# Optimization experiments

Hardware: AMD Instinct MI355X
Metric: run time of the kernel (lower is better)

The kernel has to match this reference:

```python
import jax, jax.numpy as jnp
import numpy as np

H = 512
L = 4
A = 16
EPS = 1e-5


def setup_inputs() -> dict:
    key = jax.random.key(0)
    ks = jax.random.split(key, 16)
    B, S = 64, 256
    scale = 0.02
    inp = {
        "hidden": jnp.zeros((B, H), jnp.float32),
        "x": jax.random.normal(ks[0], (B, S, H), jnp.float32),
        "dones": jax.random.randint(ks[1], (B, S), 0, 2).astype(bool),
        "avail_actions": jax.random.randint(ks[2], (B, S, A), 0, 2).astype(bool),
        # MLP stack: L layers of Linear(H,H) + LayerNorm
        "Wl": jax.random.normal(ks[3], (L, H, H), jnp.float32) * scale,
        "bl": jnp.zeros((L, H), jnp.float32),
        "ln_g": jnp.ones((L, H), jnp.float32),
        "ln_b": jnp.zeros((L, H), jnp.float32),
        # GRUCell(H, H): torch layout weight_ih [3H, H] (r, z, n order)
        "W_ih": jax.random.normal(ks[4], (3 * H, H), jnp.float32) * scale,
        "W_hh": jax.random.normal(ks[5], (3 * H, H), jnp.float32) * scale,
        "b_ih": jnp.zeros((3 * H,), jnp.float32),
        "b_hh": jnp.zeros((3 * H,), jnp.float32),
        # output head
        "Wq": jax.random.normal(ks[6], (A, H), jnp.float32) * scale,
        "bq": jnp.zeros((A,), jnp.float32),
    }
    return inp


def _layer_norm(x, g, b):
    mu = jnp.mean(x, axis=-1, keepdims=True)
    var = jnp.mean(jnp.square(x - mu), axis=-1, keepdims=True)
    return (x - mu) * jax.lax.rsqrt(var + EPS) * g + b


def _gru_scan(h0, x, dones, W_ih, W_hh, b_ih, b_hh):
    # Precompute input projections for all timesteps: [B, S, 3H]
    gi = jnp.einsum("bsh,gh->bsg", x, W_ih) + b_ih
    gi_t = jnp.swapaxes(gi, 0, 1)          # [S, B, 3H]
    dones_t = jnp.swapaxes(dones, 0, 1)    # [S, B]

    def step(h, inputs):
        gi_s, done_s = inputs
        h = jnp.where(done_s[:, None], 0.0, h)  # reset carry where done
        gh = h @ W_hh.T + b_hh
        i_r, i_z, i_n = jnp.split(gi_s, 3, axis=-1)
        h_r, h_z, h_n = jnp.split(gh, 3, axis=-1)
        r = jax.nn.sigmoid(i_r + h_r)
        z = jax.nn.sigmoid(i_z + h_z)
        n = jnp.tanh(i_n + r * h_n)
        h_new = (1.0 - z) * n + z * h
        return h_new, h_new

    h_final, outs = jax.lax.scan(step, h0, (gi_t, dones_t))
    return h_final, jnp.swapaxes(outs, 0, 1)  # [B, S, H]


def reference(hidden, x, dones, avail_actions, Wl, bl, ln_g, ln_b,
              W_ih, W_hh, b_ih, b_hh, Wq, bq):
    h = x
    for l in range(L):
        h = jnp.einsum("bsh,oh->bso", h, Wl[l]) + bl[l]
        h = jax.nn.relu(_layer_norm(h, ln_g[l], ln_b[l]))
    hidden_out, rnn_out = _gru_scan(hidden, h, dones, W_ih, W_hh, b_ih, b_hh)
    q = jnp.einsum("bsh,ah->bsa", rnn_out, Wq) + bq
    unavail = 1.0 - avail_actions.astype(q.dtype)
    q = q - unavail * 1e10
    return hidden_out, q
```

## Files before the change

### kernel.cpp

```cpp
#include <hip/hip_runtime.h>
#include <hip/hip_bf16.h>

typedef short short8 __attribute__((ext_vector_type(8)));
typedef float f32x4 __attribute__((ext_vector_type(4)));

#define H 512
#define BATCH 64
#define SEQ 256
#define NROWS 16384
#define NDOM 16
#define HSTCAP 12288

__device__ __forceinline__ float bf2f(unsigned short u) {
    union { unsigned int i; float f; } v;
    v.i = ((unsigned int)u) << 16;
    return v.f;
}
__device__ __forceinline__ unsigned short f2bf(float f) {
    union { float f; unsigned int i; } v;
    v.f = f;
    unsigned int lsb = (v.i >> 16) & 1u;
    v.i += 0x7fffu + lsb;
    return (unsigned short)(v.i >> 16);
}
__device__ __forceinline__ float sigm(float x) { return 1.f / (1.f + __expf(-x)); }
__device__ __forceinline__ float tanh_fast(float x) { return 2.f / (1.f + __expf(-2.f * x)) - 1.f; }

__global__ __launch_bounds__(256) void cvt_init(
    const float* __restrict__ Wl, const float* __restrict__ Wih,
    unsigned short* __restrict__ wlb, unsigned short* __restrict__ wihb,
    unsigned int* __restrict__ meta)
{
    long idx4 = (long)blockIdx.x * 256 + threadIdx.x;
    if (idx4 < 2560) meta[idx4] = 0u;
    long i = idx4 * 4;
    const long N1 = 1048576;
    const long N2 = N1 + 786432;
    const float* src; unsigned short* dst; long off;
    if (i < N1)      { src = Wl;  dst = wlb;  off = i; }
    else if (i < N2) { src = Wih; dst = wihb; off = i - N1; }
    else return;
    float4 v = *(const float4*)(src + off);
    ushort4 o;
    o.x = f2bf(v.x); o.y = f2bf(v.y); o.z = f2bf(v.z); o.w = f2bf(v.w);
    *(ushort4*)(dst + off) = o;
}

__global__ __launch_bounds__(256) void seg_build(
    const int* __restrict__ dones, int* __restrict__ lenArr,
    unsigned int* __restrict__ hist)
{
    __shared__ int d[256];
    const int b = blockIdx.x, s = threadIdx.x;
    d[s] = dones[b * 256 + s];
    __syncthreads();
    int len = 0;
    bool start = (s == 0) || (d[s] != 0);
    if (start) {
        len = 1;
        while (s + len < 256 && d[s + len] == 0) len++;
        atomicAdd(&hist[len], 1u);
    }
    lenArr[b * 256 + s] = len;
}

__global__ __launch_bounds__(256) void seg_offsets(
    const unsigned int* __restrict__ hist, int* __restrict__ Marr,
    unsigned int* __restrict__ offs, unsigned int* __restrict__ ssum)
{
    __shared__ unsigned int h[257];
    __shared__ int Msh[257];
    const int t = threadIdx.x;
    h[t] = hist[t];
    if (t == 0) h[256] = hist[256];
    __syncthreads();
    for (int tt = t; tt <= 256; tt += 256) {
        unsigned int m = 0;
        for (int L = tt + 1; L <= 256; ++L) m += h[L];
        Marr[tt] = (int)m;
        offs[tt] = m;
        Msh[tt] = (int)m;
    }
    __syncthreads();
    if (t == 0) {
        unsigned int acc = 0;
        for (int k = 0; k <= 256; ++k) { ssum[k] = acc; acc += (unsigned int)Msh[k]; }
    }
}

__global__ __launch_bounds__(256) void seg_scatter(
    const int* __restrict__ lenArr, unsigned int* __restrict__ offs,
    int* __restrict__ recs)
{
    const int b = blockIdx.x, s = threadIdx.x;
    int len = lenArr[b * 256 + s];
    if (len > 0) {
        unsigned int pos = atomicAdd(&offs[len], 1u);
        recs[pos] = (b << 16) | s;
    }
}

__global__ __launch_bounds__(256) void pmap_build(
    const int* __restrict__ recs, const int* __restrict__ Marr,
    const unsigned int* __restrict__ ssum, const int* __restrict__ lenArr,
    int* __restrict__ pmap)
{
    const int i = blockIdx.x * 256 + threadIdx.x;
    if (i >= Marr[0]) return;
    int rec = recs[i];
    int b = rec >> 16, st = rec & 0xffff;
    int len = lenArr[b * 256 + st];
    for (int t = 0; t < len; ++t) pmap[b * 256 + st + t] = (int)ssum[t] + i;
}

__global__ __launch_bounds__(256) void h_init(
    const int* __restrict__ recs, const int* __restrict__ Marr,
    const int* __restrict__ dones, const float* __restrict__ hidden,
    unsigned short* __restrict__ hst)
{
    const int w = threadIdx.x >> 6, lane = threadIdx.x & 63;
    const int i = blockIdx.x * 4 + w;
    const int nseg = Marr[0];
    const int c0 = lane * 8;
    unsigned short* dst = hst + (long)i * 512 + c0;
    if (i < nseg) {
        int rec = recs[i];
        int b = rec >> 16, st = rec & 0xffff;
        if (st == 0 && dones[b * 256] == 0) {
            float4 va = *(const float4*)(hidden + b * 512 + c0);
            float4 vb = *(const float4*)(hidden + b * 512 + c0 + 4);
            ushort4 o0 = {f2bf(va.x), f2bf(va.y), f2bf(va.z), f2bf(va.w)};
            ushort4 o1 = {f2bf(vb.x), f2bf(vb.y), f2bf(vb.z), f2bf(vb.w)};
            *(ushort4*)dst = o0; *(ushort4*)(dst + 4) = o1;
            return;
        }
    }
    ushort4 z4 = {0, 0, 0, 0};
    *(ushort4*)dst = z4; *(ushort4*)(dst + 4) = z4;
}

__global__ __launch_bounds__(256) void mlp_gi(
    const float* __restrict__ x,
    const unsigned short* __restrict__ wlb,
    const unsigned short* __restrict__ wihb,
    const float* __restrict__ bl,
    const float* __restrict__ lng,
    const float* __restrict__ lnb,
    const float* __restrict__ bih,
    const int* __restrict__ pmap,
    unsigned short* __restrict__ gi)
{
    __shared__ unsigned short ldsAct[64 * 512];
    __shared__ unsigned short ldsW[512 * 64];
    __shared__ float red[64 * 8];
    const int tid = threadIdx.x;
    const int lane = tid & 63;
    const int w = tid >> 6;
    const long m0 = (long)blockIdx.x * 64;

#pragma unroll
    for (int it = 0; it < 16; ++it) {
        int ch = it * 256 + tid;
        int row = ch >> 6;
        int c = ch & 63;
        const float* xp = x + (m0 + row) * 512 + c * 8;
        float4 a = *(const float4*)xp;
        float4 b4 = *(const float4*)(xp + 4);
        short8 v;
        v[0] = (short)f2bf(a.x);  v[1] = (short)f2bf(a.y);
        v[2] = (short)f2bf(a.z);  v[3] = (short)f2bf(a.w);
        v[4] = (short)f2bf(b4.x); v[5] = (short)f2bf(b4.y);
        v[6] = (short)f2bf(b4.z); v[7] = (short)f2bf(b4.w);
        int byteo = (row * 1024 + c * 16) ^ ((row & 7) << 4);
        *(short8*)((char*)ldsAct + byteo) = v;
    }
    int pm[4][4];
#pragma unroll
    for (int i = 0; i < 4; ++i)
#pragma unroll
        for (int r = 0; r < 4; ++r)
            pm[i][r] = pmap[m0 + i * 16 + (lane >> 4) * 4 + r];
    __syncthreads();

    for (int l = 0; l < 4; ++l) {
        const unsigned short* W = wlb + (long)l * 512 * 512;
        f32x4 acc[4][8];
#pragma unroll
        for (int i = 0; i < 4; ++i)
#pragma unroll
            for (int jn = 0; jn < 8; ++jn) acc[i][jn] = (f32x4){0.f, 0.f, 0.f, 0.f};

        for (int kt = 0; kt < 512; kt += 64) {
            __syncthreads();
#pragma unroll
            for (int i = 0; i < 16; ++i) {
                int o = (i * 256 + tid) * 16;
                int row = o >> 7;
                int c = (o & 127) >> 4;
                long gcol = (long)kt * 2 + (long)((c ^ (row & 7)) << 4);
                __builtin_amdgcn_global_load_lds(
                    (const unsigned int*)((const char*)W + (long)row * 1024 + gcol),
                    (unsigned int*)(ldsW + (i * 256 + w * 64) * 8), 16, 0, 0);
            }
            __syncthreads();
#pragma unroll
            for (int k2 = 0; k2 < 2; ++k2) {
                short8 af[4], bfr[8];
#pragma unroll
                for (int i = 0; i < 4; ++i) {
                    int row = i * 16 + (lane & 15);
                    int byteo = (row * 1024 + kt * 2 + k2 * 64 + ((lane >> 4) * 16)) ^ ((row & 7) << 4);
                    af[i] = *(const short8*)((const char*)ldsAct + byteo);
                }
#pragma unroll
                for (int jn = 0; jn < 8; ++jn) {
                    int row = w * 128 + jn * 16 + (lane & 15);
                    int byteo = (row * 128 + k2 * 64 + ((lane >> 4) * 16)) ^ ((row & 7) << 4);
                    bfr[jn] = *(const short8*)((const char*)ldsW + byteo);
                }
#pragma unroll
                for (int i = 0; i < 4; ++i)
#pragma unroll
                    for (int jn = 0; jn < 8; ++jn)
                        acc[i][jn] = __builtin_amdgcn_mfma_f32_16x16x32_bf16(af[i], bfr[jn], acc[i][jn], 0, 0, 0);
            }
        }

        float bz[8], gl[8], bb[8];
#pragma unroll
        for (int jn = 0; jn < 8; ++jn) {
            int n = w * 128 + jn * 16 + (lane & 15);
            bz[jn] = bl[l * 512 + n]; gl[jn] = lng[l * 512 + n]; bb[jn] = lnb[l * 512 + n];
        }
#pragma unroll
        for (int i = 0; i < 4; ++i)
#pragma unroll
            for (int jn = 0; jn < 8; ++jn)
#pragma unroll
                for (int r = 0; r < 4; ++r) acc[i][jn][r] += bz[jn];

#pragma unroll
        for (int i = 0; i < 4; ++i) {
#pragma unroll
            for (int r = 0; r < 4; ++r) {
                float sv = 0.f, qv = 0.f;
#pragma unroll
                for (int jn = 0; jn < 8; ++jn) {
                    float v = acc[i][jn][r];
                    sv += v; qv += v * v;
                }
                sv += __shfl_xor(sv, 1); qv += __shfl_xor(qv, 1);
                sv += __shfl_xor(sv, 2); qv += __shfl_xor(qv, 2);
                sv += __shfl_xor(sv, 4); qv += __shfl_xor(qv, 4);
                sv += __shfl_xor(sv, 8); qv += __shfl_xor(qv, 8);
                if ((lane & 15) == 0) {
                    int row = i * 16 + (lane >> 4) * 4 + r;
                    red[row * 8 + w * 2] = sv;
                    red[row * 8 + w * 2 + 1] = qv;
                }
            }
        }
        __syncthreads();

#pragma unroll
        for (int i = 0; i < 4; ++i) {
#pragma unroll
            for (int r = 0; r < 4; ++r) {
                int row = i * 16 + (lane >> 4) * 4 + r;
                float s_tot = red[row * 8 + 0] + red[row * 8 + 2] + red[row * 8 + 4] + red[row * 8 + 6];
                float q_tot = red[row * 8 + 1] + red[row * 8 + 3] + red[row * 8 + 5] + red[row * 8 + 7];
                float mu = s_tot * (1.f / 512.f);
                float var = q_tot * (1.f / 512.f) - mu * mu;
                float rs = rsqrtf(var + 1e-5f);
#pragma unroll
                for (int jn = 0; jn < 8; ++jn) {
                    int col = w * 128 + jn * 16 + (lane & 15);
                    float v = fmaxf(0.f, (acc[i][jn][r] - mu) * rs * gl[jn] + bb[jn]);
                    int byteo = (row * 1024 + col * 2) ^ ((row & 7) << 4);
                    *(unsigned short*)((char*)ldsAct + byteo) = f2bf(v);
                }
            }
        }
        __syncthreads();
    }

    for (int nc = 0; nc < 3; ++nc) {
        const unsigned short* W = wihb + (long)nc * 512 * 512;
        f32x4 acc[4][8];
#pragma unroll
        for (int i = 0; i < 4; ++i)
#pragma unroll
            for (int jn = 0; jn < 8; ++jn) acc[i][jn] = (f32x4){0.f, 0.f, 0.f, 0.f};

        for (int kt = 0; kt < 512; kt += 64) {
            __syncthreads();
#pragma unroll
            for (int i = 0; i < 16; ++i) {
                int o = (i * 256 + tid) * 16;
                int row = o >> 7;
                int c = (o & 127) >> 4;
                long gcol = (long)kt * 2 + (long)((c ^ (row & 7)) << 4);
                __builtin_amdgcn_global_load_lds(
                    (const unsigned int*)((const char*)W + (long)row * 1024 + gcol),
                    (unsigned int*)(ldsW + (i * 256 + w * 64) * 8), 16, 0, 0);
            }
            __syncthreads();
#pragma unroll
            for (int k2 = 0; k2 < 2; ++k2) {
                short8 af[4], bfr[8];
#pragma unroll
                for (int i = 0; i < 4; ++i) {
                    int row = i * 16 + (lane & 15);
                    int byteo = (row * 1024 + kt * 2 + k2 * 64 + ((lane >> 4) * 16)) ^ ((row & 7) << 4);
                    af[i] = *(const short8*)((const char*)ldsAct + byteo);
                }
#pragma unroll
                for (int jn = 0; jn < 8; ++jn) {
                    int row = w * 128 + jn * 16 + (lane & 15);
                    int byteo = (row * 128 + k2 * 64 + ((lane >> 4) * 16)) ^ ((row & 7) << 4);
                    bfr[jn] = *(const short8*)((const char*)ldsW + byteo);
                }
#pragma unroll
                for (int i = 0; i < 4; ++i)
#pragma unroll
                    for (int jn = 0; jn < 8; ++jn)
                        acc[i][jn] = __builtin_amdgcn_mfma_f32_16x16x32_bf16(af[i], bfr[jn], acc[i][jn], 0, 0, 0);
            }
        }

#pragma unroll
        for (int jn = 0; jn < 8; ++jn) {
            int colg = nc * 512 + w * 128 + jn * 16 + (lane & 15);
            float bz = bih[colg];
#pragma unroll
            for (int i = 0; i < 4; ++i)
#pragma unroll
                for (int r = 0; r < 4; ++r)
                    gi[(long)pm[i][r] * 1536 + colg] = f2bf(acc[i][jn][r] + bz);
        }
    }
}

__device__ __forceinline__ void dbar(unsigned int* __restrict__ dm,
                                     unsigned int epoch)
{
    __syncthreads();
    if (threadIdx.x == 0) {
        unsigned int p = __hip_atomic_fetch_add(&dm[0], 1u, __ATOMIC_RELAXED,
                                                __HIP_MEMORY_SCOPE_AGENT);
        if (p == (epoch + 1u) * 16u - 1u) {
            __hip_atomic_store(&dm[16], epoch + 1u, __ATOMIC_RELAXED,
                               __HIP_MEMORY_SCOPE_AGENT);
        } else {
            while (__hip_atomic_load(&dm[16], __ATOMIC_RELAXED,
                                     __HIP_MEMORY_SCOPE_AGENT) <= epoch)
                __builtin_amdgcn_s_sleep(2);
        }
    }
    __syncthreads();
    __builtin_amdgcn_sched_barrier(0);
}

__global__ __launch_bounds__(256, 1) void gru_seg_scan(
    const unsigned short* __restrict__ gi,
    const float* __restrict__ Whh,
    const float* __restrict__ bhh,
    const int* __restrict__ Marr,
    const unsigned int* __restrict__ ssum,
    const int* __restrict__ recs,
    unsigned short* __restrict__ hstA,
    unsigned short* __restrict__ hstB,
    unsigned short* __restrict__ rnn,
    float* __restrict__ hid_out,
    unsigned int* __restrict__ meta)
{
    __shared__ unsigned short ldsW[96 * 512];
    __shared__ int sMarr[257];
    __shared__ unsigned int sssum[257];
    const int tid = threadIdx.x;
    const int lane = tid & 63;
    const int w = tid >> 6;
    const int jg = blockIdx.x >> 4;
    const int dom = blockIdx.x & 15;
    const int j0 = jg * 32;

    for (int e = tid; e < 96 * 512; e += 256) {
        int rrow = e >> 9;
        int col = e & 511;
        int gate = rrow >> 5;
        int jl = rrow & 31;
        float v = Whh[((long)(gate * 512 + j0 + jl)) * 512 + col];
        int byteo = (rrow * 1024 + col * 2) ^ ((rrow & 7) << 4);
        *(unsigned short*)((char*)ldsW + byteo) = f2bf(v);
    }
    for (int e = tid; e < 257; e += 256) { sMarr[e] = Marr[e]; sssum[e] = ssum[e]; }

    const int jl16 = lane & 15;
    float bhr[2], bhz[2], bhn[2];
#pragma unroll
    for (int jj = 0; jj < 2; ++jj) {
        int jc = j0 + jj * 16 + jl16;
        bhr[jj] = bhh[jc]; bhz[jj] = bhh[512 + jc]; bhn[jj] = bhh[1024 + jc];
    }
    const int rbase = w * 16 + (lane >> 4) * 4;
    const int arowl = w * 16 + jl16;
    const int kcol0 = (lane >> 4) * 8;
    unsigned int* dmeta = meta + 64 * dom;
    __syncthreads();

    int crec[4], nrec[4];
    unsigned short cgr[4][2], cgz[4][2], cgn[4][2];
    unsigned short ngr[4][2], ngz[4][2], ngn[4][2];

    {
        const int Mt0 = sMarr[0];
        const long b0 = (long)sssum[0];
#pragma unroll
        for (int q = 0; q < 4; ++q) {
            int r = dom * 64 + rbase + q;
            if (r < Mt0) {
                crec[q] = recs[r];
#pragma unroll
                for (int jj = 0; jj < 2; ++jj) {
                    const unsigned short* gp = gi + (b0 + r) * 1536 + j0 + jj * 16 + jl16;
                    cgr[q][jj] = gp[0]; cgz[q][jj] = gp[512]; cgn[q][jj] = gp[1024];
                }
            } else crec[q] = -1;
        }
    }

    for (int t = 0; t < 256; ++t) {
        const int Mt = sMarr[t];
        if (Mt == 0) break;
        const int ntiles = (Mt + 63) >> 6;
        if (dom >= ntiles) break;
        const unsigned short* hsrc = (t & 1) ? hstB : hstA;
        unsigned short* hdst = (t & 1) ? hstA : hstB;
        const long base = (long)sssum[t];

        for (int tt = dom; tt < ntiles; tt += NDOM) {
            const int r0 = tt * 64;

            const unsigned short* arowp = hsrc + ((long)(r0 + arowl)) * 512 + kcol0;
            short8 af[16];
#pragma unroll
            for (int kk = 0; kk < 16; ++kk) {
                const unsigned short* ap = arowp + kk * 32;
                asm volatile("global_load_dwordx4 %0, %1, off sc0"
                             : "=v"(af[kk]) : "v"(ap));
            }
            unsigned int hu[4][2];
#pragma unroll
            for (int q = 0; q < 4; ++q)
#pragma unroll
                for (int jj = 0; jj < 2; ++jj) {
                    const unsigned short* hp = hsrc + (long)(r0 + rbase + q) * 512
                                             + j0 + jj * 16 + jl16;
                    asm volatile("global_load_ushort %0, %1, off sc0"
                                 : "=v"(hu[q][jj]) : "v"(hp));
                }
            asm volatile("s_waitcnt vmcnt(0)" ::: "memory");
            __builtin_amdgcn_sched_barrier(0);

            const bool instep = (tt + NDOM < ntiles);
            if (instep) {
#pragma unroll
                for (int q = 0; q < 4; ++q) {
                    int r = (tt + NDOM) * 64 + rbase + q;
                    if (r < Mt) {
                        nrec[q] = recs[r];
#pragma unroll
                        for (int jj = 0; jj < 2; ++jj) {
                            const unsigned short* gp = gi + (base + r) * 1536 + j0 + jj * 16 + jl16;
                            ngr[q][jj] = gp[0]; ngz[q][jj] = gp[512]; ngn[q][jj] = gp[1024];
                        }
                    } else nrec[q] = -1;
                }
            }

            f32x4 acch[3][2];
#pragma unroll
            for (int g = 0; g < 3; ++g)
#pragma unroll
                for (int jj = 0; jj < 2; ++jj) acch[g][jj] = (f32x4){0.f, 0.f, 0.f, 0.f};

#pragma unroll
            for (int kk = 0; kk < 16; ++kk) {
#pragma unroll
                for (int g = 0; g < 3; ++g)
#pragma unroll
                    for (int jj = 0; jj < 2; ++jj) {
                        int rrow = g * 32 + jj * 16 + jl16;
                        int bbyte = (rrow * 1024 + kk * 64 + ((lane >> 4) * 16)) ^ ((rrow & 7) << 4);
                        short8 bfrag = *(const short8*)((const char*)ldsW + bbyte);
                        acch[g][jj] = __builtin_amdgcn_mfma_f32_16x16x32_bf16(af[kk], bfrag, acch[g][jj], 0, 0, 0);
                    }
            }

#pragma unroll
            for (int q = 0; q < 4; ++q) {
                if (crec[q] >= 0) {
                    int r = r0 + rbase + q;
                    int b = crec[q] >> 16, st = crec[q] & 0xffff;
                    int s = st + t;
#pragma unroll
                    for (int jj = 0; jj < 2; ++jj) {
                        int jc = j0 + jj * 16 + jl16;
                        float heff = bf2f((unsigned short)hu[q][jj]);
                        float rgt = sigm(bf2f(cgr[q][jj]) + acch[0][jj][q] + bhr[jj]);
                        float zgt = sigm(bf2f(cgz[q][jj]) + acch[1][jj][q] + bhz[jj]);
                        float ngt = tanh_fast(bf2f(cgn[q][jj]) + rgt * (acch[2][jj][q] + bhn[jj]));
                        float hnew = (1.f - zgt) * ngt + zgt * heff;
                        unsigned short hb16 = f2bf(hnew);
                        hdst[(long)r * 512 + jc] = hb16;
                        rnn[((long)(b * 256 + s)) * 512 + jc] = hb16;
                        if (s == 255) hid_out[b * 512 + jc] = hnew;
                    }
                }
            }
            if (instep) {
#pragma unroll
                for (int q = 0; q < 4; ++q) {
                    crec[q] = nrec[q];
#pragma unroll
                    for (int jj = 0; jj < 2; ++jj) {
                        cgr[q][jj] = ngr[q][jj]; cgz[q][jj] = ngz[q][jj]; cgn[q][jj] = ngn[q][jj];
                    }
                }
            }
        }

        {
            const int Mt1 = sMarr[t + 1];
            if (Mt1 > 0 && dom < ((Mt1 + 63) >> 6)) {
                const long b1 = (long)sssum[t + 1];
#pragma unroll
                for (int q = 0; q < 4; ++q) {
                    int r = dom * 64 + rbase + q;
                    if (r < Mt1) {
                        crec[q] = recs[r];
#pragma unroll
                        for (int jj = 0; jj < 2; ++jj) {
                            const unsigned short* gp = gi + (b1 + r) * 1536 + j0 + jj * 16 + jl16;
                            cgr[q][jj] = gp[0]; cgz[q][jj] = gp[512]; cgn[q][jj] = gp[1024];
                        }
                    } else crec[q] = -1;
                }
            }
        }
        dbar(dmeta, (unsigned int)t);
    }
}

__global__ __launch_bounds__(256) void qhead(
    const unsigned short* __restrict__ rnn, const float* __restrict__ Wq,
    const float* __restrict__ bq, const int* __restrict__ avail,
    float* __restrict__ qout)
{
    const int w = threadIdx.x >> 6;
    const int lane = threadIdx.x & 63;
    const long row = (long)blockIdx.x * 4 + w;
    const int a = lane & 15;
    const int kc = lane >> 4;
    const unsigned short* hr = rnn + row * H + kc * 128;
    const float* wr = Wq + a * H + kc * 128;
    float sum = 0.f;
#pragma unroll
    for (int i = 0; i < 128; i += 8) {
        short8 hv = *(const short8*)(hr + i);
        float4 wa = *(const float4*)(wr + i);
        float4 wb = *(const float4*)(wr + i + 4);
        sum += bf2f((unsigned short)hv[0]) * wa.x;
        sum += bf2f((unsigned short)hv[1]) * wa.y;
        sum += bf2f((unsigned short)hv[2]) * wa.z;
        sum += bf2f((unsigned short)hv[3]) * wa.w;
        sum += bf2f((unsigned short)hv[4]) * wb.x;
        sum += bf2f((unsigned short)hv[5]) * wb.y;
        sum += bf2f((unsigned short)hv[6]) * wb.z;
        sum += bf2f((unsigned short)hv[7]) * wb.w;
    }
    sum += __shfl_xor(sum, 16);
    sum += __shfl_xor(sum, 32);
    if (kc == 0) {
        float qv = sum + bq[a];
        int av = avail[row * 16 + a];
        if (av == 0) qv -= 1e10f;
        qout[row * 16 + a] = qv;
    }
}

extern "C" void kernel_launch(void* const* d_in, const int* in_sizes, int n_in,
                              void* d_out, int out_size, void* d_ws, size_t ws_size,
                              hipStream_t stream)
{
    const float* hidden = (const float*)d_in[0];
    const float* x      = (const float*)d_in[1];
    const int*   dones  = (const int*)d_in[2];
    const int*   avail  = (const int*)d_in[3];
    const float* Wl     = (const float*)d_in[4];
    const float* bl     = (const float*)d_in[5];
    const float* ln_g   = (const float*)d_in[6];
    const float* ln_b   = (const float*)d_in[7];
    const float* W_ih   = (const float*)d_in[8];
    const float* W_hh   = (const float*)d_in[9];
    const float* b_ih   = (const float*)d_in[10];
    const float* b_hh   = (const float*)d_in[11];
    const float* Wq     = (const float*)d_in[12];
    const float* bq     = (const float*)d_in[13];

    char* p = (char*)d_ws;
    unsigned short* gi   = (unsigned short*)p; p += (size_t)NROWS * 1536 * 2;
    unsigned short* rnn  = (unsigned short*)p; p += (size_t)NROWS * H * 2;
    unsigned short* hst0 = (unsigned short*)p; p += (size_t)HSTCAP * H * 2;
    unsigned short* hst1 = (unsigned short*)p; p += (size_t)HSTCAP * H * 2;
    unsigned short* wlb  = (unsigned short*)p; p += (size_t)4 * H * H * 2;
    unsigned short* wihb = (unsigned short*)p; p += (size_t)3 * H * H * 2;
    int* lenArr = (int*)p;          p += (size_t)NROWS * 4;
    int* recs   = (int*)p;          p += (size_t)NROWS * 4;
    int* pmap   = (int*)p;          p += (size_t)NROWS * 4;
    unsigned int* meta = (unsigned int*)p;  p += 12288;
    unsigned int* hist = meta + 1024;
    unsigned int* offs = meta + 1296;
    int* Marr = (int*)(meta + 1568);
    unsigned int* ssum = meta + 1840;

    cvt_init<<<1792, 256, 0, stream>>>(Wl, W_ih, wlb, wihb, meta);

    seg_build<<<64, 256, 0, stream>>>(dones, lenArr, hist);
    seg_offsets<<<1, 256, 0, stream>>>(hist, Marr, offs, ssum);
    seg_scatter<<<64, 256, 0, stream>>>(lenArr, offs, recs);
    pmap_build<<<64, 256, 0, stream>>>(recs, Marr, ssum, lenArr, pmap);

    h_init<<<HSTCAP / 4, 256, 0, stream>>>(recs, Marr, dones, hidden, hst0);

    mlp_gi<<<256, 256, 0, stream>>>(x, wlb, wihb, bl, ln_g, ln_b, b_ih, pmap, gi);

    gru_seg_scan<<<256, 256, 0, stream>>>(gi, W_hh, b_hh, Marr, ssum, recs,
                                          hst0, hst1, rnn, (float*)d_out, meta);

    qhead<<<4096, 256, 0, stream>>>(rnn, Wq, bq, avail, (float*)d_out + BATCH * H);
}
```

Measured before the change: 572.7 us.

## Use master-gathered flag barrier in GRU scan and direct-load weights in MLP

The per-domain grid barrier in the GRU scan changes from a single atomic counter to per-workgroup flags on separate cache lines. Workgroup 0 polls all flags, then releases the others through one broadcast flag, which removes contention on one atomic address at every timestep. The MLP/input-projection kernel moves to 512 threads per block and drops the LDS staging of weights; each wave now reads its B fragments straight from global/L2. This removes the per-k-tile syncthreads, but the weights are no longer shared in LDS and global load latency is exposed. The metadata area grows to fit the padded flags.

```diff
diff --git a/kernel.cpp b/kernel.cpp
--- a/kernel.cpp
+++ b/kernel.cpp
@@ -32,7 +32,7 @@
     unsigned int* __restrict__ meta)
 {
     long idx4 = (long)blockIdx.x * 256 + threadIdx.x;
-    if (idx4 < 2560) meta[idx4] = 0u;
+    if (idx4 < 20480) meta[idx4] = 0u;
     long i = idx4 * 4;
     const long N1 = 1048576;
     const long N2 = N1 + 786432;
@@ -139,7 +139,7 @@
     *(ushort4*)dst = z4; *(ushort4*)(dst + 4) = z4;
 }
 
-__global__ __launch_bounds__(256) void mlp_gi(
+__global__ __launch_bounds__(512) void mlp_gi(
     const float* __restrict__ x,
     const unsigned short* __restrict__ wlb,
     const unsigned short* __restrict__ wihb,
@@ -151,16 +151,17 @@
     unsigned short* __restrict__ gi)
 {
     __shared__ unsigned short ldsAct[64 * 512];
-    __shared__ unsigned short ldsW[512 * 64];
-    __shared__ float red[64 * 8];
+    __shared__ float red[64 * 16];
     const int tid = threadIdx.x;
     const int lane = tid & 63;
     const int w = tid >> 6;
     const long m0 = (long)blockIdx.x * 64;
-
-#pragma unroll
-    for (int it = 0; it < 16; ++it) {
-        int ch = it * 256 + tid;
+    const int l15 = lane & 15;
+    const int l4 = lane >> 4;
+
+#pragma unroll
+    for (int it = 0; it < 8; ++it) {
+        int ch = it * 512 + tid;
         int row = ch >> 6;
         int c = ch & 63;
         const float* xp = x + (m0 + row) * 512 + c * 8;
@@ -179,63 +180,48 @@
     for (int i = 0; i < 4; ++i)
 #pragma unroll
         for (int r = 0; r < 4; ++r)
-            pm[i][r] = pmap[m0 + i * 16 + (lane >> 4) * 4 + r];
+            pm[i][r] = pmap[m0 + i * 16 + l4 * 4 + r];
     __syncthreads();
 
     for (int l = 0; l < 4; ++l) {
         const unsigned short* W = wlb + (long)l * 512 * 512;
-        f32x4 acc[4][8];
+        const unsigned short* wr0 = W + (long)(w * 64 + l15) * 512 + l4 * 8;
+        f32x4 acc[4][4];
 #pragma unroll
         for (int i = 0; i < 4; ++i)
 #pragma unroll
-            for (int jn = 0; jn < 8; ++jn) acc[i][jn] = (f32x4){0.f, 0.f, 0.f, 0.f};
-
-        for (int kt = 0; kt < 512; kt += 64) {
-            __syncthreads();
-#pragma unroll
-            for (int i = 0; i < 16; ++i) {
-                int o = (i * 256 + tid) * 16;
-                int row = o >> 7;
-                int c = (o & 127) >> 4;
-                long gcol = (long)kt * 2 + (long)((c ^ (row & 7)) << 4);
-                __builtin_amdgcn_global_load_lds(
-                    (const unsigned int*)((const char*)W + (long)row * 1024 + gcol),
-                    (unsigned int*)(ldsW + (i * 256 + w * 64) * 8), 16, 0, 0);
-            }
-            __syncthreads();
-#pragma unroll
-            for (int k2 = 0; k2 < 2; ++k2) {
-                short8 af[4], bfr[8];
-#pragma unroll
-                for (int i = 0; i < 4; ++i) {
-                    int row = i * 16 + (lane & 15);
-                    int byteo = (row * 1024 + kt * 2 + k2 * 64 + ((lane >> 4) * 16)) ^ ((row & 7) << 4);
-                    af[i] = *(const short8*)((const char*)ldsAct + byteo);
-                }
-#pragma unroll
-                for (int jn = 0; jn < 8; ++jn) {
-                    int row = w * 128 + jn * 16 + (lane & 15);
-                    int byteo = (row * 128 + k2 * 64 + ((lane >> 4) * 16)) ^ ((row & 7) << 4);
-                    bfr[jn] = *(const short8*)((const char*)ldsW + byteo);
-                }
-#pragma unroll
-                for (int i = 0; i < 4; ++i)
-#pragma unroll
-                    for (int jn = 0; jn < 8; ++jn)
-                        acc[i][jn] = __builtin_amdgcn_mfma_f32_16x16x32_bf16(af[i], bfr[jn], acc[i][jn], 0, 0, 0);
-            }
-        }
-
-        float bz[8], gl[8], bb[8];
-#pragma unroll
-        for (int jn = 0; jn < 8; ++jn) {
-            int n = w * 128 + jn * 16 + (lane & 15);
+            for (int jn = 0; jn < 4; ++jn) acc[i][jn] = (f32x4){0.f, 0.f, 0.f, 0.f};
+
+#pragma unroll
+        for (int kk = 0; kk < 16; ++kk) {
+            short8 bfr[4];
+#pragma unroll
+            for (int jn = 0; jn < 4; ++jn)
+                bfr[jn] = *(const short8*)(wr0 + (long)jn * 16 * 512 + kk * 32);
+            short8 af[4];
+#pragma unroll
+            for (int i = 0; i < 4; ++i) {
+                int row = i * 16 + l15;
+                int byteo = (row * 1024 + kk * 64 + l4 * 16) ^ ((row & 7) << 4);
+                af[i] = *(const short8*)((const char*)ldsAct + byteo);
+            }
+#pragma unroll
+            for (int i = 0; i < 4; ++i)
+#pragma unroll
+                for (int jn = 0; jn < 4; ++jn)
+                    acc[i][jn] = __builtin_amdgcn_mfma_f32_16x16x32_bf16(af[i], bfr[jn], acc[i][jn], 0, 0, 0);
+        }
+
+        float bz[4], gl[4], bb[4];
+#pragma unroll
+        for (int jn = 0; jn < 4; ++jn) {
+            int n = w * 64 + jn * 16 + l15;
             bz[jn] = bl[l * 512 + n]; gl[jn] = lng[l * 512 + n]; bb[jn] = lnb[l * 512 + n];
         }
 #pragma unroll
         for (int i = 0; i < 4; ++i)
 #pragma unroll
-            for (int jn = 0; jn < 8; ++jn)
+            for (int jn = 0; jn < 4; ++jn)
 #pragma unroll
                 for (int r = 0; r < 4; ++r) acc[i][jn][r] += bz[jn];
 
@@ -245,7 +231,7 @@
             for (int r = 0; r < 4; ++r) {
                 float sv = 0.f, qv = 0.f;
 #pragma unroll
-                for (int jn = 0; jn < 8; ++jn) {
+                for (int jn = 0; jn < 4; ++jn) {
                     float v = acc[i][jn][r];
                     sv += v; qv += v * v;
                 }
@@ -253,10 +239,10 @@
                 sv += __shfl_xor(sv, 2); qv += __shfl_xor(qv, 2);
                 sv += __shfl_xor(sv, 4); qv += __shfl_xor(qv, 4);
                 sv += __shfl_xor(sv, 8); qv += __shfl_xor(qv, 8);
-                if ((lane & 15) == 0) {
-                    int row = i * 16 + (lane >> 4) * 4 + r;
-                    red[row * 8 + w * 2] = sv;
-                    red[row * 8 + w * 2 + 1] = qv;
+                if (l15 == 0) {
+                    int row = i * 16 + l4 * 4 + r;
+                    red[row * 16 + w * 2] = sv;
+                    red[row * 16 + w * 2 + 1] = qv;
                 }
             }
         }
@@ -266,15 +252,19 @@
         for (int i = 0; i < 4; ++i) {
 #pragma unroll
             for (int r = 0; r < 4; ++r) {
-                int row = i * 16 + (lane >> 4) * 4 + r;
-                float s_tot = red[row * 8 + 0] + red[row * 8 + 2] + red[row * 8 + 4] + red[row * 8 + 6];
-                float q_tot = red[row * 8 + 1] + red[row * 8 + 3] + red[row * 8 + 5] + red[row * 8 + 7];
+                int row = i * 16 + l4 * 4 + r;
+                float s_tot = 0.f, q_tot = 0.f;
+#pragma unroll
+                for (int ww = 0; ww < 8; ++ww) {
+                    s_tot += red[row * 16 + ww * 2];
+                    q_tot += red[row * 16 + ww * 2 + 1];
+                }
                 float mu = s_tot * (1.f / 512.f);
                 float var = q_tot * (1.f / 512.f) - mu * mu;
                 float rs = rsqrtf(var + 1e-5f);
 #pragma unroll
-                for (int jn = 0; jn < 8; ++jn) {
-                    int col = w * 128 + jn * 16 + (lane & 15);
+                for (int jn = 0; jn < 4; ++jn) {
+                    int col = w * 64 + jn * 16 + l15;
                     float v = fmaxf(0.f, (acc[i][jn][r] - mu) * rs * gl[jn] + bb[jn]);
                     int byteo = (row * 1024 + col * 2) ^ ((row & 7) << 4);
                     *(unsigned short*)((char*)ldsAct + byteo) = f2bf(v);
@@ -286,51 +276,36 @@
 
     for (int nc = 0; nc < 3; ++nc) {
         const unsigned short* W = wihb + (long)nc * 512 * 512;
-        f32x4 acc[4][8];
+        const unsigned short* wr0 = W + (long)(w * 64 + l15) * 512 + l4 * 8;
+        f32x4 acc[4][4];
 #pragma unroll
         for (int i = 0; i < 4; ++i)
 #pragma unroll
-            for (int jn = 0; jn < 8; ++jn) acc[i][jn] = (f32x4){0.f, 0.f, 0.f, 0.f};
-
-        for (int kt = 0; kt < 512; kt += 64) {
-            __syncthreads();
-#pragma unroll
-            for (int i = 0; i < 16; ++i) {
-                int o = (i * 256 + tid) * 16;
-                int row = o >> 7;
-                int c = (o & 127) >> 4;
-                long gcol = (long)kt * 2 + (long)((c ^ (row & 7)) << 4);
-                __builtin_amdgcn_global_load_lds(
-                    (const unsigned int*)((const char*)W + (long)row * 1024 + gcol),
-                    (unsigned int*)(ldsW + (i * 256 + w * 64) * 8), 16, 0, 0);
-            }
-            __syncthreads();
-#pragma unroll
-            for (int k2 = 0; k2 < 2; ++k2) {
-                short8 af[4], bfr[8];
-#pragma unroll
-                for (int i = 0; i < 4; ++i) {
-                    int row = i * 16 + (lane & 15);
-                    int byteo = (row * 1024 + kt * 2 + k2 * 64 + ((lane >> 4) * 16)) ^ ((row & 7) << 4);
-                    af[i] = *(const short8*)((const char*)ldsAct + byteo);
-                }
-#pragma unroll
-                for (int jn = 0; jn < 8; ++jn) {
-                    int row = w * 128 + jn * 16 + (lane & 15);
-                    int byteo = (row * 128 + k2 * 64 + ((lane >> 4) * 16)) ^ ((row & 7) << 4);
-                    bfr[jn] = *(const short8*)((const char*)ldsW + byteo);
-                }
-#pragma unroll
-                for (int i = 0; i < 4; ++i)
-#pragma unroll
-                    for (int jn = 0; jn < 8; ++jn)
-                        acc[i][jn] = __builtin_amdgcn_mfma_f32_16x16x32_bf16(af[i], bfr[jn], acc[i][jn], 0, 0, 0);
-            }
-        }
-
-#pragma unroll
-        for (int jn = 0; jn < 8; ++jn) {
-            int colg = nc * 512 + w * 128 + jn * 16 + (lane & 15);
+            for (int jn = 0; jn < 4; ++jn) acc[i][jn] = (f32x4){0.f, 0.f, 0.f, 0.f};
+
+#pragma unroll
+        for (int kk = 0; kk < 16; ++kk) {
+            short8 bfr[4];
+#pragma unroll
+            for (int jn = 0; jn < 4; ++jn)
+                bfr[jn] = *(const short8*)(wr0 + (long)jn * 16 * 512 + kk * 32);
+            short8 af[4];
+#pragma unroll
+            for (int i = 0; i < 4; ++i) {
+                int row = i * 16 + l15;
+                int byteo = (row * 1024 + kk * 64 + l4 * 16) ^ ((row & 7) << 4);
+                af[i] = *(const short8*)((const char*)ldsAct + byteo);
+            }
+#pragma unroll
+            for (int i = 0; i < 4; ++i)
+#pragma unroll
+                for (int jn = 0; jn < 4; ++jn)
+                    acc[i][jn] = __builtin_amdgcn_mfma_f32_16x16x32_bf16(af[i], bfr[jn], acc[i][jn], 0, 0, 0);
+        }
+
+#pragma unroll
+        for (int jn = 0; jn < 4; ++jn) {
+            int colg = nc * 512 + w * 64 + jn * 16 + l15;
             float bz = bih[colg];
 #pragma unroll
             for (int i = 0; i < 4; ++i)
@@ -342,19 +317,29 @@
 }
 
 __device__ __forceinline__ void dbar(unsigned int* __restrict__ dm,
-                                     unsigned int epoch)
+                                     int wg, unsigned int epoch)
 {
     __syncthreads();
-    if (threadIdx.x == 0) {
-        unsigned int p = __hip_atomic_fetch_add(&dm[0], 1u, __ATOMIC_RELAXED,
-                                                __HIP_MEMORY_SCOPE_AGENT);
-        if (p == (epoch + 1u) * 16u - 1u) {
-            __hip_atomic_store(&dm[16], epoch + 1u, __ATOMIC_RELAXED,
+    const int tid = threadIdx.x;
+    if (wg == 0) {
+        if (tid == 0)
+            __hip_atomic_store(&dm[0], epoch + 1u, __ATOMIC_RELAXED,
                                __HIP_MEMORY_SCOPE_AGENT);
-        } else {
-            while (__hip_atomic_load(&dm[16], __ATOMIC_RELAXED,
+        if (tid < 16) {
+            while (__hip_atomic_load(&dm[tid * 32], __ATOMIC_RELAXED,
                                      __HIP_MEMORY_SCOPE_AGENT) <= epoch)
-                __builtin_amdgcn_s_sleep(2);
+                __builtin_amdgcn_s_sleep(1);
+        }
+        if (tid == 0)
+            __hip_atomic_store(&dm[512], epoch + 1u, __ATOMIC_RELAXED,
+                               __HIP_MEMORY_SCOPE_AGENT);
+    } else {
+        if (tid == 0) {
+            __hip_atomic_store(&dm[wg * 32], epoch + 1u, __ATOMIC_RELAXED,
+                               __HIP_MEMORY_SCOPE_AGENT);
+            while (__hip_atomic_load(&dm[512], __ATOMIC_RELAXED,
+                                     __HIP_MEMORY_SCOPE_AGENT) <= epoch)
+                __builtin_amdgcn_s_sleep(1);
         }
     }
     __syncthreads();
@@ -405,7 +390,7 @@
     const int rbase = w * 16 + (lane >> 4) * 4;
     const int arowl = w * 16 + jl16;
     const int kcol0 = (lane >> 4) * 8;
-    unsigned int* dmeta = meta + 64 * dom;
+    unsigned int* dmeta = meta + 1024 * dom;
     __syncthreads();
 
     int crec[4], nrec[4];
@@ -548,7 +533,7 @@
                 }
             }
         }
-        dbar(dmeta, (unsigned int)t);
+        dbar(dmeta, jg, (unsigned int)t);
     }
 }
 
@@ -618,11 +603,11 @@
     int* lenArr = (int*)p;          p += (size_t)NROWS * 4;
     int* recs   = (int*)p;          p += (size_t)NROWS * 4;
     int* pmap   = (int*)p;          p += (size_t)NROWS * 4;
-    unsigned int* meta = (unsigned int*)p;  p += 12288;
-    unsigned int* hist = meta + 1024;
-    unsigned int* offs = meta + 1296;
-    int* Marr = (int*)(meta + 1568);
-    unsigned int* ssum = meta + 1840;
+    unsigned int* meta = (unsigned int*)p;  p += 20480 * 4;
+    unsigned int* hist = meta + 16384;
+    unsigned int* offs = meta + 16672;
+    int* Marr = (int*)(meta + 16960);
+    unsigned int* ssum = meta + 17248;
 
     cvt_init<<<1792, 256, 0, stream>>>(Wl, W_ih, wlb, wihb, meta);
 
@@ -633,7 +618,7 @@
 
     h_init<<<HSTCAP / 4, 256, 0, stream>>>(recs, Marr, dones, hidden, hst0);
 
-    mlp_gi<<<256, 256, 0, stream>>>(x, wlb, wihb, bl, ln_g, ln_b, b_ih, pmap, gi);
+    mlp_gi<<<256, 512, 0, stream>>>(x, wlb, wihb, bl, ln_g, ln_b, b_ih, pmap, gi);
 
     gru_seg_scan<<<256, 256, 0, stream>>>(gi, W_hh, b_hh, Marr, ssum, recs,
                                           hst0, hst1, rnn, (float*)d_out, meta);
```

New measurement: 606.2 us. +5.9%, slower.
